# Optimization experiments

Measured on AMD Instinct MI355X. Metric: run time of the kernel, lower is better.

Reference implementation:

```python
import jax, jax.numpy as jnp
import numpy as np

N_NODES = 50000
N_EDGES = 800000
D_IN = 128
D_OUT = 128
K = 3


def setup_inputs() -> dict:
    key = jax.random.key(0)
    k1, k2, k3, k4 = jax.random.split(key, 4)
    x = jax.random.normal(k1, (N_NODES, D_IN), dtype=jnp.float32)
    W = jax.random.normal(k2, (K, D_IN, D_OUT), dtype=jnp.float32) * 0.05
    edge_index = jax.random.randint(k3, (K, 2, N_EDGES), 0, N_NODES, dtype=jnp.int32)
    edge_weight = jax.random.uniform(k4, (K, N_EDGES), dtype=jnp.float32)
    return {"x": x, "W": W, "edge_index": edge_index, "edge_weight": edge_weight}


def reference(x, W, edge_index, edge_weight):
    # ChebConv: out = sum_k A_k @ (x @ W_k), A_k given as weighted edge lists.
    n = x.shape[0]
    out = jnp.zeros((n, W.shape[-1]), dtype=x.dtype)
    for k in range(W.shape[0]):
        h = x @ W[k]                                   # [N, D_OUT] dense GEMM
        src = edge_index[k, 0]
        dst = edge_index[k, 1]
        msg = h[src] * edge_weight[k][:, None]         # [E, D_OUT] gather + scale
        out = out + jax.ops.segment_sum(msg, dst, num_segments=n)
    return out
```

## Files before the change

### kernel.cpp

```cpp
#include <hip/hip_runtime.h>
#include <hip/hip_bf16.h>

#define N_NODES 50000
#define N_EDGES 800000
#define D 128
#define KCHEB 3
#define NBKT 98
#define TOTB (KCHEB * NBKT)
#define SLAB 16384
#define EPB 4096
#define NBLK_E ((N_EDGES + EPB - 1) / EPB)

typedef __attribute__((ext_vector_type(8))) short short8v;
typedef __attribute__((ext_vector_type(4))) float f32x4;

__device__ inline unsigned f2bf(float f) {
    unsigned x = __float_as_uint(f);
    unsigned r = ((x >> 16) & 1u) + 0x7FFFu;
    return (x + r) >> 16;
}

__global__ __launch_bounds__(256) void wprep(const float* __restrict__ W,
                                             unsigned short* __restrict__ Wtg,
                                             int* __restrict__ cursor) {
    const int k = blockIdx.x;
    if (k == 0)
        for (int i = threadIdx.x; i < TOTB; i += 256) cursor[i] = 0;
    const float* Wk = W + (size_t)k * D * D;
    unsigned short* o = Wtg + (size_t)k * D * D;
    for (int i = threadIdx.x; i < 4096; i += 256) {
        int r  = i >> 5;
        int c4 = (i & 31) * 4;
        float4 wv = *(const float4*)&Wk[r * 128 + c4];
        #pragma unroll
        for (int j = 0; j < 4; ++j) {
            int row = c4 + j;
            int byte_in_row = (r * 2) ^ ((row & 7) << 4);
            o[row * 128 + (byte_in_row >> 1)] = (unsigned short)f2bf((&wv.x)[j]);
        }
    }
}

__global__ __launch_bounds__(256) void gemm_mfma(const float* __restrict__ x,
                                                 const unsigned short* __restrict__ Wtg,
                                                 unsigned* __restrict__ h3, int n) {
    __shared__ unsigned short Wt[128 * 128];
    const int t = threadIdx.x;
    unsigned* h2 = h3 + (size_t)blockIdx.y * N_NODES * 64;

    {
        const uint4* src = (const uint4*)(Wtg + (size_t)blockIdx.y * D * D);
        uint4* dst = (uint4*)Wt;
        #pragma unroll
        for (int i = 0; i < 8; ++i) dst[t + 256 * i] = src[t + 256 * i];
    }
    __syncthreads();

    const int lane = t & 63, w = t >> 6;
    const int m0 = blockIdx.x * 64 + w * 16;
    const int arow = m0 + (lane & 15);
    const float* xr = x + (size_t)(arow < n ? arow : 0) * D + ((lane >> 4) << 3);

    short8v afr[4];
    #pragma unroll
    for (int kt = 0; kt < 4; ++kt) {
        float4 p0 = *(const float4*)(xr + kt * 32);
        float4 p1 = *(const float4*)(xr + kt * 32 + 4);
        union { short8v s; unsigned u[4]; } a;
        a.u[0] = f2bf(p0.x) | (f2bf(p0.y) << 16);
        a.u[1] = f2bf(p0.z) | (f2bf(p0.w) << 16);
        a.u[2] = f2bf(p1.x) | (f2bf(p1.y) << 16);
        a.u[3] = f2bf(p1.z) | (f2bf(p1.w) << 16);
        afr[kt] = a.s;
    }

    f32x4 acc[8] = {};
    const int kb = (lane >> 4) << 4;
    #pragma unroll
    for (int nn = 0; nn < 8; ++nn) {
        const int row = nn * 16 + (lane & 15);
        const int sw = (row & 7) << 4;
        const unsigned short* wr = &Wt[row * 128];
        #pragma unroll
        for (int kt = 0; kt < 4; ++kt) {
            int byte_in_row = ((kt << 6) + kb) ^ sw;
            short8v b = *(const short8v*)&wr[byte_in_row >> 1];
            acc[nn] = __builtin_amdgcn_mfma_f32_16x16x32_bf16(b, afr[kt], acc[nn], 0, 0, 0);
        }
    }

    const int node = m0 + (lane & 15);
    if (node < n) {
        unsigned short* hs = (unsigned short*)h2;
        const int g4 = (lane >> 4) << 2;
        #pragma unroll
        for (int nn = 0; nn < 8; ++nn) {
            unsigned lo = f2bf(acc[nn][0]) | (f2bf(acc[nn][1]) << 16);
            unsigned hi = f2bf(acc[nn][2]) | (f2bf(acc[nn][3]) << 16);
            *(uint2*)&hs[(size_t)node * D + nn * 16 + g4] = make_uint2(lo, hi);
        }
    }
}

__global__ __launch_bounds__(1024) void bucket_bin(const int* __restrict__ ei,
                                                   const float* __restrict__ ew,
                                                   int* __restrict__ cursor,
                                                   uint2* __restrict__ binned) {
    __shared__ int lh[NBKT], gb[NBKT], lc[NBKT];
    const int k = blockIdx.y, t = threadIdx.x;
    for (int i = t; i < NBKT; i += 1024) { lh[i] = 0; lc[i] = 0; }
    __syncthreads();
    const int* srcs = ei + (size_t)k * 2 * N_EDGES;
    const int* dsts = srcs + N_EDGES;
    const float* w = ew + (size_t)k * N_EDGES;
    const int e = blockIdx.x * EPB + t * 4;
    const bool ok = e < N_EDGES;

    int4 d4 = make_int4(0, 0, 0, 0), s4 = make_int4(0, 0, 0, 0);
    float4 w4 = make_float4(0.f, 0.f, 0.f, 0.f);
    if (ok) {
        d4 = *(const int4*)&dsts[e];
        s4 = *(const int4*)&srcs[e];
        w4 = *(const float4*)&w[e];
        atomicAdd(&lh[d4.x >> 9], 1);
        atomicAdd(&lh[d4.y >> 9], 1);
        atomicAdd(&lh[d4.z >> 9], 1);
        atomicAdd(&lh[d4.w >> 9], 1);
    }
    __syncthreads();
    for (int i = t; i < NBKT; i += 1024)
        gb[i] = lh[i] ? atomicAdd(&cursor[k * NBKT + i], lh[i]) : 0;
    __syncthreads();
    if (ok) {
        #pragma unroll
        for (int j = 0; j < 4; ++j) {
            int d = (&d4.x)[j];
            int b = d >> 9;
            int pos = (k * NBKT + b) * SLAB + gb[b] + atomicAdd(&lc[b], 1);
            binned[pos] = make_uint2(__float_as_uint((&w4.x)[j]),
                                     (unsigned)(&s4.x)[j] | ((unsigned)(d & 511) << 16));
        }
    }
}

__global__ __launch_bounds__(1024) void build_csr(const uint2* __restrict__ binned,
                                                  const int* __restrict__ cursor,
                                                  int* __restrict__ off,
                                                  int* __restrict__ num,
                                                  unsigned* __restrict__ csr4) {
    __shared__ int nh[512], ex[512], wsum[4];
    const int kb = blockIdx.x;
    const int k = kb / NBKT, b = kb % NBKT;
    const int t = threadIdx.x;
    const int beg = kb * SLAB;
    const int end = beg + cursor[kb];

    for (int i = t; i < 512; i += 1024) nh[i] = 0;
    __syncthreads();
    for (int i = beg + t; i < end; i += 1024)
        atomicAdd(&nh[(binned[i].y >> 16) & 511], 1);
    __syncthreads();

    if (t < 256) {
        int a0 = nh[2 * t], a1 = nh[2 * t + 1];
        int s = a0 + a1;
        int lane = t & 63, wid = t >> 6;
        int v = s;
        #pragma unroll
        for (int d = 1; d < 64; d <<= 1) {
            int u = __shfl_up(v, d, 64);
            if (lane >= d) v += u;
        }
        if (lane == 63) wsum[wid] = v;
        __syncthreads();
        int wb = 0;
        for (int i = 0; i < wid; ++i) wb += wsum[i];
        int ep = wb + v - s;
        ex[2 * t] = ep;
        ex[2 * t + 1] = ep + a0;

        const int node0 = b * 512;
        int n0 = node0 + 2 * t, n1 = node0 + 2 * t + 1;
        if (n0 < N_NODES) { off[k * N_NODES + n0] = beg + ep;      num[k * N_NODES + n0] = a0; }
        if (n1 < N_NODES) { off[k * N_NODES + n1] = beg + ep + a0; num[k * N_NODES + n1] = a1; }
    } else {
        __syncthreads();
    }
    for (int i = t; i < 512; i += 1024) nh[i] = 0;
    __syncthreads();
    for (int i = beg + t; i < end; i += 1024) {
        uint2 e = binned[i];
        int dl = (e.y >> 16) & 511;
        int pos = beg + ex[dl] + atomicAdd(&nh[dl], 1);
        csr4[pos] = (e.y & 0xFFFFu) | (f2bf(__uint_as_float(e.x)) << 16);
    }
}

__global__ __launch_bounds__(256) void gather_all(const unsigned* __restrict__ h3,
                                                  const unsigned* __restrict__ csr4,
                                                  const int* __restrict__ off,
                                                  const int* __restrict__ num,
                                                  float* __restrict__ out) {
    const int half = threadIdx.x >> 5;
    const int l = threadIdx.x & 31;
    const int node = blockIdx.x * 8 + half;
    if (node >= N_NODES) return;

    float a0 = 0.f, a1 = 0.f, a2 = 0.f, a3 = 0.f;
    #pragma unroll
    for (int k = 0; k < KCHEB; ++k) {
        const unsigned* h2 = h3 + (size_t)k * N_NODES * 64;
        const int kd = k * N_NODES + node;
        const int i0 = off[kd];
        const int cnt = num[kd];
        for (int b0 = 0; b0 < cnt; b0 += 8) {
            unsigned e[8];
            uint2 u[8];
            float wv[8];
            #pragma unroll
            for (int j = 0; j < 8; ++j) {
                bool okj = (b0 + j) < cnt;
                e[j] = csr4[okj ? i0 + b0 + j : i0];
                wv[j] = okj ? __uint_as_float(e[j] & 0xFFFF0000u) : 0.f;
            }
            #pragma unroll
            for (int j = 0; j < 8; ++j)
                u[j] = *(const uint2*)&h2[(size_t)(e[j] & 0xFFFFu) * 64 + l * 2];
            #pragma unroll
            for (int j = 0; j < 8; ++j) {
                a0 += wv[j] * __uint_as_float(u[j].x << 16);
                a1 += wv[j] * __uint_as_float(u[j].x & 0xFFFF0000u);
                a2 += wv[j] * __uint_as_float(u[j].y << 16);
                a3 += wv[j] * __uint_as_float(u[j].y & 0xFFFF0000u);
            }
        }
    }
    *(float4*)&out[(size_t)node * D + l * 4] = make_float4(a0, a1, a2, a3);
}

extern "C" void kernel_launch(void* const* d_in, const int* in_sizes, int n_in,
                              void* d_out, int out_size, void* d_ws, size_t ws_size,
                              hipStream_t stream) {
    const float* x  = (const float*)d_in[0];
    const float* W  = (const float*)d_in[1];
    const int*   ei = (const int*)d_in[2];
    const float* ew = (const float*)d_in[3];
    float* out = (float*)d_out;

    char* ws = (char*)d_ws;
    unsigned*       csr4   = (unsigned*)      (ws);
    uint2*          binned = (uint2*)         (ws + 19267584);
    unsigned*       h3     = (unsigned*)      (ws + 57802752);
    int*            off    = (int*)           (ws + 96202752);
    int*            num    = (int*)           (ws + 96802752);
    int*            cursor = (int*)           (ws + 97402752);
    unsigned short* Wtg    = (unsigned short*)(ws + 97403936);

    wprep<<<KCHEB, 256, 0, stream>>>(W, Wtg, cursor);

    const dim3 egrid(NBLK_E, KCHEB);
    bucket_bin<<<egrid, 1024, 0, stream>>>(ei, ew, cursor, binned);

    const dim3 ggrid((N_NODES + 63) / 64, KCHEB);
    gemm_mfma<<<ggrid, 256, 0, stream>>>(x, Wtg, h3, N_NODES);

    build_csr<<<TOTB, 1024, 0, stream>>>(binned, cursor, off, num, csr4);

    const int gat_grid = (N_NODES + 7) / 8;
    gather_all<<<gat_grid, 256, 0, stream>>>(h3, csr4, off, num, out);
}
```

Baseline: 251.0 us.

## Fuse edge binning and GEMM into one interleaved kernel launch

Merges the bucket-binning and MFMA GEMM kernels into a single launch whose even blocks run the GEMM tiles (now 128 rows, 512 threads) and odd blocks bin edge chunks (now 2048 edges each). The two independent stages can then overlap on the GPU and one launch boundary disappears. The gather's padded index now points at the last valid CSR entry rather than the first, which keeps the loads local. The risk is that the larger shared LDS footprint and mixed block types lower occupancy or balance the work unevenly.

```diff
diff --git a/kernel.cpp b/kernel.cpp
--- a/kernel.cpp
+++ b/kernel.cpp
@@ -8,8 +8,9 @@
 #define NBKT 98
 #define TOTB (KCHEB * NBKT)
 #define SLAB 16384
-#define EPB 4096
-#define NBLK_E ((N_EDGES + EPB - 1) / EPB)
+#define EPB 2048
+#define NCHUNK ((N_EDGES + EPB - 1) / EPB)
+#define NMT ((N_NODES + 127) / 128)
 
 typedef __attribute__((ext_vector_type(8))) short short8v;
 typedef __attribute__((ext_vector_type(4))) float f32x4;
@@ -41,104 +42,112 @@
     }
 }
 
-__global__ __launch_bounds__(256) void gemm_mfma(const float* __restrict__ x,
-                                                 const unsigned short* __restrict__ Wtg,
-                                                 unsigned* __restrict__ h3, int n) {
-    __shared__ unsigned short Wt[128 * 128];
+__global__ __launch_bounds__(512) void pack_bin_gemm(const int* __restrict__ ei,
+                                                     const float* __restrict__ ew,
+                                                     int* __restrict__ cursor,
+                                                     uint2* __restrict__ binned,
+                                                     const float* __restrict__ x,
+                                                     const unsigned short* __restrict__ Wtg,
+                                                     unsigned* __restrict__ h3, int n) {
+    __shared__ unsigned char lds[32768];
     const int t = threadIdx.x;
-    unsigned* h2 = h3 + (size_t)blockIdx.y * N_NODES * 64;
-
-    {
-        const uint4* src = (const uint4*)(Wtg + (size_t)blockIdx.y * D * D);
-        uint4* dst = (uint4*)Wt;
-        #pragma unroll
-        for (int i = 0; i < 8; ++i) dst[t + 256 * i] = src[t + 256 * i];
-    }
-    __syncthreads();
-
-    const int lane = t & 63, w = t >> 6;
-    const int m0 = blockIdx.x * 64 + w * 16;
-    const int arow = m0 + (lane & 15);
-    const float* xr = x + (size_t)(arow < n ? arow : 0) * D + ((lane >> 4) << 3);
-
-    short8v afr[4];
-    #pragma unroll
-    for (int kt = 0; kt < 4; ++kt) {
-        float4 p0 = *(const float4*)(xr + kt * 32);
-        float4 p1 = *(const float4*)(xr + kt * 32 + 4);
-        union { short8v s; unsigned u[4]; } a;
-        a.u[0] = f2bf(p0.x) | (f2bf(p0.y) << 16);
-        a.u[1] = f2bf(p0.z) | (f2bf(p0.w) << 16);
-        a.u[2] = f2bf(p1.x) | (f2bf(p1.y) << 16);
-        a.u[3] = f2bf(p1.z) | (f2bf(p1.w) << 16);
-        afr[kt] = a.s;
-    }
-
-    f32x4 acc[8] = {};
-    const int kb = (lane >> 4) << 4;
-    #pragma unroll
-    for (int nn = 0; nn < 8; ++nn) {
-        const int row = nn * 16 + (lane & 15);
-        const int sw = (row & 7) << 4;
-        const unsigned short* wr = &Wt[row * 128];
+    const int gid = blockIdx.x >> 1;
+
+    if ((blockIdx.x & 1) == 0) {
+        unsigned short* Wt = (unsigned short*)lds;
+        const int kc = gid / NMT;
+        const int mt = gid % NMT;
+        unsigned* h2 = h3 + (size_t)kc * N_NODES * 64;
+        {
+            const uint4* src = (const uint4*)(Wtg + (size_t)kc * D * D);
+            uint4* dst = (uint4*)Wt;
+            #pragma unroll
+            for (int i = 0; i < 4; ++i) dst[t + 512 * i] = src[t + 512 * i];
+        }
+        __syncthreads();
+
+        const int lane = t & 63, w = t >> 6;
+        const int m0 = mt * 128 + w * 16;
+        const int arow = m0 + (lane & 15);
+        const float* xr = x + (size_t)(arow < n ? arow : 0) * D + ((lane >> 4) << 3);
+
+        short8v afr[4];
         #pragma unroll
         for (int kt = 0; kt < 4; ++kt) {
-            int byte_in_row = ((kt << 6) + kb) ^ sw;
-            short8v b = *(const short8v*)&wr[byte_in_row >> 1];
-            acc[nn] = __builtin_amdgcn_mfma_f32_16x16x32_bf16(b, afr[kt], acc[nn], 0, 0, 0);
-        }
-    }
-
-    const int node = m0 + (lane & 15);
-    if (node < n) {
-        unsigned short* hs = (unsigned short*)h2;
-        const int g4 = (lane >> 4) << 2;
+            float4 p0 = *(const float4*)(xr + kt * 32);
+            float4 p1 = *(const float4*)(xr + kt * 32 + 4);
+            union { short8v s; unsigned u[4]; } a;
+            a.u[0] = f2bf(p0.x) | (f2bf(p0.y) << 16);
+            a.u[1] = f2bf(p0.z) | (f2bf(p0.w) << 16);
+            a.u[2] = f2bf(p1.x) | (f2bf(p1.y) << 16);
+            a.u[3] = f2bf(p1.z) | (f2bf(p1.w) << 16);
+            afr[kt] = a.s;
+        }
+
+        f32x4 acc[8] = {};
+        const int kb = (lane >> 4) << 4;
         #pragma unroll
         for (int nn = 0; nn < 8; ++nn) {
-            unsigned lo = f2bf(acc[nn][0]) | (f2bf(acc[nn][1]) << 16);
-            unsigned hi = f2bf(acc[nn][2]) | (f2bf(acc[nn][3]) << 16);
-            *(uint2*)&hs[(size_t)node * D + nn * 16 + g4] = make_uint2(lo, hi);
-        }
-    }
-}
-
-__global__ __launch_bounds__(1024) void bucket_bin(const int* __restrict__ ei,
-                                                   const float* __restrict__ ew,
-                                                   int* __restrict__ cursor,
-                                                   uint2* __restrict__ binned) {
-    __shared__ int lh[NBKT], gb[NBKT], lc[NBKT];
-    const int k = blockIdx.y, t = threadIdx.x;
-    for (int i = t; i < NBKT; i += 1024) { lh[i] = 0; lc[i] = 0; }
-    __syncthreads();
-    const int* srcs = ei + (size_t)k * 2 * N_EDGES;
-    const int* dsts = srcs + N_EDGES;
-    const float* w = ew + (size_t)k * N_EDGES;
-    const int e = blockIdx.x * EPB + t * 4;
-    const bool ok = e < N_EDGES;
-
-    int4 d4 = make_int4(0, 0, 0, 0), s4 = make_int4(0, 0, 0, 0);
-    float4 w4 = make_float4(0.f, 0.f, 0.f, 0.f);
-    if (ok) {
-        d4 = *(const int4*)&dsts[e];
-        s4 = *(const int4*)&srcs[e];
-        w4 = *(const float4*)&w[e];
-        atomicAdd(&lh[d4.x >> 9], 1);
-        atomicAdd(&lh[d4.y >> 9], 1);
-        atomicAdd(&lh[d4.z >> 9], 1);
-        atomicAdd(&lh[d4.w >> 9], 1);
-    }
-    __syncthreads();
-    for (int i = t; i < NBKT; i += 1024)
-        gb[i] = lh[i] ? atomicAdd(&cursor[k * NBKT + i], lh[i]) : 0;
-    __syncthreads();
-    if (ok) {
-        #pragma unroll
-        for (int j = 0; j < 4; ++j) {
-            int d = (&d4.x)[j];
-            int b = d >> 9;
-            int pos = (k * NBKT + b) * SLAB + gb[b] + atomicAdd(&lc[b], 1);
-            binned[pos] = make_uint2(__float_as_uint((&w4.x)[j]),
-                                     (unsigned)(&s4.x)[j] | ((unsigned)(d & 511) << 16));
+            const int row = nn * 16 + (lane & 15);
+            const int sw = (row & 7) << 4;
+            const unsigned short* wr = &Wt[row * 128];
+            #pragma unroll
+            for (int kt = 0; kt < 4; ++kt) {
+                int byte_in_row = ((kt << 6) + kb) ^ sw;
+                short8v b = *(const short8v*)&wr[byte_in_row >> 1];
+                acc[nn] = __builtin_amdgcn_mfma_f32_16x16x32_bf16(b, afr[kt], acc[nn], 0, 0, 0);
+            }
+        }
+
+        const int node = m0 + (lane & 15);
+        if (node < n) {
+            unsigned short* hs = (unsigned short*)h2;
+            const int g4 = (lane >> 4) << 2;
+            #pragma unroll
+            for (int nn = 0; nn < 8; ++nn) {
+                unsigned lo = f2bf(acc[nn][0]) | (f2bf(acc[nn][1]) << 16);
+                unsigned hi = f2bf(acc[nn][2]) | (f2bf(acc[nn][3]) << 16);
+                *(uint2*)&hs[(size_t)node * D + nn * 16 + g4] = make_uint2(lo, hi);
+            }
+        }
+    } else {
+        int* lh = (int*)lds;
+        int* gb = lh + NBKT;
+        int* lc = gb + NBKT;
+        const int k = gid / NCHUNK;
+        const int chunk = gid % NCHUNK;
+        for (int i = t; i < NBKT; i += 512) { lh[i] = 0; lc[i] = 0; }
+        __syncthreads();
+        const int* srcs = ei + (size_t)k * 2 * N_EDGES;
+        const int* dsts = srcs + N_EDGES;
+        const float* w = ew + (size_t)k * N_EDGES;
+        const int e = chunk * EPB + t * 4;
+        const bool ok = e < N_EDGES;
+
+        int4 d4 = make_int4(0, 0, 0, 0), s4 = make_int4(0, 0, 0, 0);
+        float4 w4 = make_float4(0.f, 0.f, 0.f, 0.f);
+        if (ok) {
+            d4 = *(const int4*)&dsts[e];
+            s4 = *(const int4*)&srcs[e];
+            w4 = *(const float4*)&w[e];
+            atomicAdd(&lh[d4.x >> 9], 1);
+            atomicAdd(&lh[d4.y >> 9], 1);
+            atomicAdd(&lh[d4.z >> 9], 1);
+            atomicAdd(&lh[d4.w >> 9], 1);
+        }
+        __syncthreads();
+        for (int i = t; i < NBKT; i += 512)
+            gb[i] = lh[i] ? atomicAdd(&cursor[k * NBKT + i], lh[i]) : 0;
+        __syncthreads();
+        if (ok) {
+            #pragma unroll
+            for (int j = 0; j < 4; ++j) {
+                int d = (&d4.x)[j];
+                int b = d >> 9;
+                int pos = (k * NBKT + b) * SLAB + gb[b] + atomicAdd(&lc[b], 1);
+                binned[pos] = make_uint2(__float_as_uint((&w4.x)[j]),
+                                         (unsigned)(&s4.x)[j] | ((unsigned)(d & 511) << 16));
+            }
         }
     }
 }
@@ -220,7 +229,7 @@
             #pragma unroll
             for (int j = 0; j < 8; ++j) {
                 bool okj = (b0 + j) < cnt;
-                e[j] = csr4[okj ? i0 + b0 + j : i0];
+                e[j] = csr4[i0 + (okj ? b0 + j : cnt - 1)];
                 wv[j] = okj ? __uint_as_float(e[j] & 0xFFFF0000u) : 0.f;
             }
             #pragma unroll
@@ -258,11 +267,8 @@
 
     wprep<<<KCHEB, 256, 0, stream>>>(W, Wtg, cursor);
 
-    const dim3 egrid(NBLK_E, KCHEB);
-    bucket_bin<<<egrid, 1024, 0, stream>>>(ei, ew, cursor, binned);
-
-    const dim3 ggrid((N_NODES + 63) / 64, KCHEB);
-    gemm_mfma<<<ggrid, 256, 0, stream>>>(x, Wtg, h3, N_NODES);
+    pack_bin_gemm<<<2 * KCHEB * NMT, 512, 0, stream>>>(ei, ew, cursor, binned,
+                                                       x, Wtg, h3, N_NODES);
 
     build_csr<<<TOTB, 1024, 0, stream>>>(binned, cursor, off, num, csr4);
 
```

Measured after the change: 252.0 us. About the same (+0.4%).
